# Optimization experiments

Measured on AMD Instinct MI355X. Metric: run time of the kernel, lower is better.

## Reference

```python
import jax, jax.numpy as jnp
import numpy as np

KSIZE = 3
STRIDE = 1
NEG_INF = -jnp.inf


def semiconv_maxmin(x, kernel, stride=STRIDE):
    """Tropical (max-min) 2D convolution, 'same' padding with -inf.

    out[n,o,i,j] = max over (c,kh,kw) of min(x_pad[n,c,i*s+kh,j*s+kw], kernel[o,c,kh,kw])
    """
    N, C, H, W = x.shape
    O, _, K, _ = kernel.shape
    p = K - 1
    top = p // 2
    bottom = p - top
    xp = jnp.pad(x, ((0, 0), (0, 0), (top, bottom), (top, bottom)),
                 constant_values=NEG_INF)
    Ho = (H + p - K) // stride + 1
    Wo = (W + p - K) // stride + 1
    out = jnp.full((N, O, Ho, Wo), NEG_INF, dtype=x.dtype)
    # Unrolled loop over the K*K taps (small, fixed); vectorized over n,o,c,h,w.
    for kh in range(K):
        for kw in range(K):
            xs = xp[:, :, kh:kh + stride * Ho:stride, kw:kw + stride * Wo:stride]  # [N,C,Ho,Wo]
            w = kernel[:, :, kh, kw]                                # [O,C]
            cand = jnp.minimum(xs[:, None], w[None, :, :, None, None])  # [N,O,C,Ho,Wo]
            out = jnp.maximum(out, jnp.max(cand, axis=2))
    return out


def setup_inputs() -> dict:
    key = jax.random.key(0)
    k1, k2 = jax.random.split(key)
    x = jax.random.normal(k1, (8, 32, 112, 112), dtype=jnp.float32)
    kernel = jax.random.normal(k2, (32, 32, KSIZE, KSIZE), dtype=jnp.float32)
    return {"x": x, "kernel": kernel}


def reference(x, kernel):
    return semiconv_maxmin(x, kernel, STRIDE)
```

## Files before the change

### kernel.cpp

```cpp
#include <hip/hip_runtime.h>
#include <math.h>

#define C_IN  32
#define O_OUT 32
#define HIMG  112
#define WIMG  112
#define HW    (HIMG * WIMG)
#define TS    8
#define NCP   16
#define XROW  12
#define XPLANE (10 * XROW)
#define WSLOT 12
#define OSTRIDE 196
#define NW    (O_OUT * NCP * WSLOT)

typedef _Float16 h2 __attribute__((ext_vector_type(2)));

static __device__ __forceinline__ h2 h2min(h2 a, h2 b) {
    return __builtin_elementwise_min(a, b);
}
static __device__ __forceinline__ h2 h2max(h2 a, h2 b) {
    return __builtin_elementwise_max(a, b);
}
static __device__ __forceinline__ h2 asH2(float f) {
    union { float f; h2 h; } u; u.f = f; return u.h;
}

__global__ void prep_weights(const float* __restrict__ kern, h2* __restrict__ wp)
{
    int idx = blockIdx.x * 256 + threadIdx.x;
    if (idx >= NW) return;
    int k  = idx % WSLOT;
    int cp = (idx / WSLOT) & (NCP - 1);
    int o  = idx / (WSLOT * NCP);
    float a = -INFINITY, b = -INFINITY;
    if (k < 9) {
        a = kern[(o * C_IN + 2 * cp    ) * 9 + k];
        b = kern[(o * C_IN + 2 * cp + 1) * 9 + k];
    }
    h2 v; v.x = (_Float16)a; v.y = (_Float16)b;
    wp[idx] = v;
}

__global__ __launch_bounds__(256, 4) void semiconv_kernel(
    const float* __restrict__ x, const h2* __restrict__ wp,
    float* __restrict__ out)
{
    __shared__ h2 xs[NCP * XPLANE];
    __shared__ h2 ws[O_OUT * OSTRIDE];

    const int tid = threadIdx.x;
    const int tj0 = blockIdx.x * TS;
    const int ti0 = blockIdx.y * TS;
    const int n   = blockIdx.z;
    const float* xn = x + (size_t)n * (C_IN * HW);

    #pragma unroll
    for (int i = 0; i < 6; ++i) {
        int chunk = i * 256 + tid;
        int o     = chunk / 48;
        int rem   = chunk - o * 48;
        float4 v  = *(const float4*)&wp[chunk * 4];
        *(float4*)&ws[o * OSTRIDE + rem * 4] = v;
    }
    #pragma unroll 1
    for (int idx = tid; idx < NCP * XPLANE; idx += 256) {
        int cp  = idx / XPLANE;
        int rem = idx - cp * XPLANE;
        int r   = rem / XROW;
        int col = rem - r * XROW;
        int gi = ti0 - 1 + r, gj = tj0 - 1 + col;
        float a = -INFINITY, b = -INFINITY;
        if (col < 10 && (unsigned)gi < (unsigned)HIMG && (unsigned)gj < (unsigned)WIMG) {
            const float* p = xn + (size_t)(2 * cp) * HW + gi * WIMG + gj;
            a = p[0];
            b = p[HW];
        }
        h2 v; v.x = (_Float16)a; v.y = (_Float16)b;
        xs[idx] = v;
    }
    __syncthreads();

    const int lane = tid & 63;
    const int wv   = tid >> 6;
    const int oL   = lane >> 3;
    const int pr   = lane & 7;
    const int o    = wv * 8 + oL;

    h2 ninf2; ninf2.x = (_Float16)(-INFINITY); ninf2.y = (_Float16)(-INFINITY);
    h2 acc[8];
    #pragma unroll
    for (int i = 0; i < 8; ++i) acc[i] = ninf2;

    #pragma unroll 2
    for (int cp = 0; cp < NCP; ++cp) {
        h2 xr[3][10];
        #pragma unroll
        for (int kh = 0; kh < 3; ++kh) {
            const h2* rp = &xs[cp * XPLANE + (pr + kh) * XROW];
            float4 a = *(const float4*)rp;
            float4 b = *(const float4*)(rp + 4);
            float2 c = *(const float2*)(rp + 8);
            xr[kh][0] = asH2(a.x); xr[kh][1] = asH2(a.y);
            xr[kh][2] = asH2(a.z); xr[kh][3] = asH2(a.w);
            xr[kh][4] = asH2(b.x); xr[kh][5] = asH2(b.y);
            xr[kh][6] = asH2(b.z); xr[kh][7] = asH2(b.w);
            xr[kh][8] = asH2(c.x); xr[kh][9] = asH2(c.y);
        }
        const h2* wq = &ws[o * OSTRIDE + cp * WSLOT];
        float4 wa = *(const float4*)wq;
        float4 wb = *(const float4*)(wq + 4);
        float  wc = *(const float*)(wq + 8);
        h2 w0 = asH2(wa.x), w1 = asH2(wa.y), w2 = asH2(wa.z), w3 = asH2(wa.w);
        h2 w4 = asH2(wb.x), w5 = asH2(wb.y), w6 = asH2(wb.z), w7 = asH2(wb.w);
        h2 w8 = asH2(wc);

        #pragma unroll
        for (int j = 0; j < 8; ++j) {
            h2 t0 = h2min(xr[0][j    ], w0);
            h2 t1 = h2min(xr[0][j + 1], w1);
            h2 t2 = h2min(xr[0][j + 2], w2);
            h2 t3 = h2min(xr[1][j    ], w3);
            h2 t4 = h2min(xr[1][j + 1], w4);
            h2 t5 = h2min(xr[1][j + 2], w5);
            h2 t6 = h2min(xr[2][j    ], w6);
            h2 t7 = h2min(xr[2][j + 1], w7);
            h2 t8 = h2min(xr[2][j + 2], w8);
            h2 r0 = h2max(h2max(t0, t1), t2);
            h2 r1 = h2max(h2max(t3, t4), t5);
            h2 r2 = h2max(h2max(t6, t7), t8);
            acc[j] = h2max(acc[j], h2max(h2max(r0, r1), r2));
        }
    }

    float* op = out + (((size_t)n * O_OUT + o) * HIMG + (ti0 + pr)) * WIMG + tj0;
    float4 v0, v1;
    v0.x = (float)(acc[0].x > acc[0].y ? acc[0].x : acc[0].y);
    v0.y = (float)(acc[1].x > acc[1].y ? acc[1].x : acc[1].y);
    v0.z = (float)(acc[2].x > acc[2].y ? acc[2].x : acc[2].y);
    v0.w = (float)(acc[3].x > acc[3].y ? acc[3].x : acc[3].y);
    v1.x = (float)(acc[4].x > acc[4].y ? acc[4].x : acc[4].y);
    v1.y = (float)(acc[5].x > acc[5].y ? acc[5].x : acc[5].y);
    v1.z = (float)(acc[6].x > acc[6].y ? acc[6].x : acc[6].y);
    v1.w = (float)(acc[7].x > acc[7].y ? acc[7].x : acc[7].y);
    *(float4*)op = v0;
    *(float4*)(op + 4) = v1;
}

extern "C" void kernel_launch(void* const* d_in, const int* in_sizes, int n_in,
                              void* d_out, int out_size, void* d_ws, size_t ws_size,
                              hipStream_t stream) {
    const float* x    = (const float*)d_in[0];
    const float* kern = (const float*)d_in[1];
    float* out        = (float*)d_out;
    h2* wp            = (h2*)d_ws;

    prep_weights<<<dim3((NW + 255) / 256), dim3(256), 0, stream>>>(kern, wp);
    dim3 grid(WIMG / TS, HIMG / TS, 8);
    semiconv_kernel<<<grid, dim3(256), 0, stream>>>(x, wp, out);
}
```

Before: 59.59 us.

## Split output channels across blocks and input channels across waves with LDS reduction

The grid is doubled so each block handles half of the output channels, which halves the weight tile in shared memory. Inside a block, the four waves are regrouped so that two waves split the input-channel pairs, and their partial max accumulators are merged through shared memory before the store. Launch bounds are raised to 8 blocks per CU for higher occupancy. The cost is that each input tile is now loaded and converted twice, once per output half, and an extra barrier and LDS round-trip are added.

```diff
diff --git a/kernel.cpp b/kernel.cpp
--- a/kernel.cpp
+++ b/kernel.cpp
@@ -12,6 +12,7 @@
 #define XPLANE (10 * XROW)
 #define WSLOT 12
 #define OSTRIDE 196
+#define OBLK  16
 #define NW    (O_OUT * NCP * WSLOT)
 
 typedef _Float16 h2 __attribute__((ext_vector_type(2)));
@@ -24,6 +25,9 @@
 }
 static __device__ __forceinline__ h2 asH2(float f) {
     union { float f; h2 h; } u; u.f = f; return u.h;
+}
+static __device__ __forceinline__ float asF(h2 h) {
+    union { h2 h; float f; } u; u.h = h; return u.f;
 }
 
 __global__ void prep_weights(const float* __restrict__ kern, h2* __restrict__ wp)
@@ -42,26 +46,27 @@
     wp[idx] = v;
 }
 
-__global__ __launch_bounds__(256, 4) void semiconv_kernel(
+__global__ __launch_bounds__(256, 8) void semiconv_kernel(
     const float* __restrict__ x, const h2* __restrict__ wp,
     float* __restrict__ out)
 {
     __shared__ h2 xs[NCP * XPLANE];
-    __shared__ h2 ws[O_OUT * OSTRIDE];
+    __shared__ h2 ws[OBLK * OSTRIDE];
 
     const int tid = threadIdx.x;
     const int tj0 = blockIdx.x * TS;
     const int ti0 = blockIdx.y * TS;
-    const int n   = blockIdx.z;
+    const int n   = blockIdx.z >> 1;
+    const int o0  = (blockIdx.z & 1) * OBLK;
     const float* xn = x + (size_t)n * (C_IN * HW);
 
     #pragma unroll
-    for (int i = 0; i < 6; ++i) {
+    for (int i = 0; i < 3; ++i) {
         int chunk = i * 256 + tid;
-        int o     = chunk / 48;
-        int rem   = chunk - o * 48;
-        float4 v  = *(const float4*)&wp[chunk * 4];
-        *(float4*)&ws[o * OSTRIDE + rem * 4] = v;
+        int oL    = chunk / 48;
+        int rem   = chunk - oL * 48;
+        float4 v  = *(const float4*)&wp[(size_t)((o0 + oL) * 48 + rem) * 4];
+        *(float4*)&ws[oL * OSTRIDE + rem * 4] = v;
     }
     #pragma unroll 1
     for (int idx = tid; idx < NCP * XPLANE; idx += 256) {
@@ -85,7 +90,10 @@
     const int wv   = tid >> 6;
     const int oL   = lane >> 3;
     const int pr   = lane & 7;
-    const int o    = wv * 8 + oL;
+    const int osl  = wv & 1;
+    const int cph  = wv >> 1;
+    const int oLoc = osl * 8 + oL;
+    const int o    = o0 + oLoc;
 
     h2 ninf2; ninf2.x = (_Float16)(-INFINITY); ninf2.y = (_Float16)(-INFINITY);
     h2 acc[8];
@@ -93,7 +101,8 @@
     for (int i = 0; i < 8; ++i) acc[i] = ninf2;
 
     #pragma unroll 2
-    for (int cp = 0; cp < NCP; ++cp) {
+    for (int ci = 0; ci < 8; ++ci) {
+        const int cp = cph * 8 + ci;
         h2 xr[3][10];
         #pragma unroll
         for (int kh = 0; kh < 3; ++kh) {
@@ -107,7 +116,7 @@
             xr[kh][6] = asH2(b.z); xr[kh][7] = asH2(b.w);
             xr[kh][8] = asH2(c.x); xr[kh][9] = asH2(c.y);
         }
-        const h2* wq = &ws[o * OSTRIDE + cp * WSLOT];
+        const h2* wq = &ws[oLoc * OSTRIDE + cp * WSLOT];
         float4 wa = *(const float4*)wq;
         float4 wb = *(const float4*)(wq + 4);
         float  wc = *(const float*)(wq + 8);
@@ -133,18 +142,40 @@
         }
     }
 
-    float* op = out + (((size_t)n * O_OUT + o) * HIMG + (ti0 + pr)) * WIMG + tj0;
-    float4 v0, v1;
-    v0.x = (float)(acc[0].x > acc[0].y ? acc[0].x : acc[0].y);
-    v0.y = (float)(acc[1].x > acc[1].y ? acc[1].x : acc[1].y);
-    v0.z = (float)(acc[2].x > acc[2].y ? acc[2].x : acc[2].y);
-    v0.w = (float)(acc[3].x > acc[3].y ? acc[3].x : acc[3].y);
-    v1.x = (float)(acc[4].x > acc[4].y ? acc[4].x : acc[4].y);
-    v1.y = (float)(acc[5].x > acc[5].y ? acc[5].x : acc[5].y);
-    v1.z = (float)(acc[6].x > acc[6].y ? acc[6].x : acc[6].y);
-    v1.w = (float)(acc[7].x > acc[7].y ? acc[7].x : acc[7].y);
-    *(float4*)op = v0;
-    *(float4*)(op + 4) = v1;
+    const int scr = oLoc * OSTRIDE + 96 + pr * 8;
+    if (cph == 1) {
+        float4 pa, pb;
+        pa.x = asF(acc[0]); pa.y = asF(acc[1]); pa.z = asF(acc[2]); pa.w = asF(acc[3]);
+        pb.x = asF(acc[4]); pb.y = asF(acc[5]); pb.z = asF(acc[6]); pb.w = asF(acc[7]);
+        *(float4*)&ws[scr]     = pa;
+        *(float4*)&ws[scr + 4] = pb;
+    }
+    __syncthreads();
+    if (cph == 0) {
+        float4 pa = *(const float4*)&ws[scr];
+        float4 pb = *(const float4*)&ws[scr + 4];
+        acc[0] = h2max(acc[0], asH2(pa.x));
+        acc[1] = h2max(acc[1], asH2(pa.y));
+        acc[2] = h2max(acc[2], asH2(pa.z));
+        acc[3] = h2max(acc[3], asH2(pa.w));
+        acc[4] = h2max(acc[4], asH2(pb.x));
+        acc[5] = h2max(acc[5], asH2(pb.y));
+        acc[6] = h2max(acc[6], asH2(pb.z));
+        acc[7] = h2max(acc[7], asH2(pb.w));
+
+        float* op = out + (((size_t)n * O_OUT + o) * HIMG + (ti0 + pr)) * WIMG + tj0;
+        float4 v0, v1;
+        v0.x = (float)(acc[0].x > acc[0].y ? acc[0].x : acc[0].y);
+        v0.y = (float)(acc[1].x > acc[1].y ? acc[1].x : acc[1].y);
+        v0.z = (float)(acc[2].x > acc[2].y ? acc[2].x : acc[2].y);
+        v0.w = (float)(acc[3].x > acc[3].y ? acc[3].x : acc[3].y);
+        v1.x = (float)(acc[4].x > acc[4].y ? acc[4].x : acc[4].y);
+        v1.y = (float)(acc[5].x > acc[5].y ? acc[5].x : acc[5].y);
+        v1.z = (float)(acc[6].x > acc[6].y ? acc[6].x : acc[6].y);
+        v1.w = (float)(acc[7].x > acc[7].y ? acc[7].x : acc[7].y);
+        *(float4*)op       = v0;
+        *(float4*)(op + 4) = v1;
+    }
 }
 
 extern "C" void kernel_launch(void* const* d_in, const int* in_sizes, int n_in,
@@ -156,6 +187,6 @@
     h2* wp            = (h2*)d_ws;
 
     prep_weights<<<dim3((NW + 255) / 256), dim3(256), 0, stream>>>(kern, wp);
-    dim3 grid(WIMG / TS, HIMG / TS, 8);
+    dim3 grid(WIMG / TS, HIMG / TS, 8 * 2);
     semiconv_kernel<<<grid, dim3(256), 0, stream>>>(x, wp, out);
 }
```

New measurement: 62.04 us. 4.1% more time.

## Split output channels across blocks and channels across waves with LDS reduction

Applied to the files above, without the earlier changes.

Each block now handles 16 output channels instead of 32, which doubles the grid along z. Within a block the four waves split the 16 input-channel pairs, and each thread computes two output rows so one set of loaded input rows is reused for both. The per-wave partial maxima are then reduced through shared memory, reusing the weight buffer. Launch bounds rise to allow 6 blocks per SM. The change adds an extra barrier and reduction step, the input tile is now loaded twice (once per output-channel half), and only wave 0 writes output.

```diff
diff --git a/kernel.cpp b/kernel.cpp
--- a/kernel.cpp
+++ b/kernel.cpp
@@ -11,7 +11,8 @@
 #define XROW  12
 #define XPLANE (10 * XROW)
 #define WSLOT 12
-#define OSTRIDE 196
+#define WSTRIDE 196
+#define OBLK  16
 #define NW    (O_OUT * NCP * WSLOT)
 
 typedef _Float16 h2 __attribute__((ext_vector_type(2)));
@@ -24,6 +25,9 @@
 }
 static __device__ __forceinline__ h2 asH2(float f) {
     union { float f; h2 h; } u; u.f = f; return u.h;
+}
+static __device__ __forceinline__ float asF(h2 h) {
+    union { h2 h; float f; } u; u.h = h; return u.f;
 }
 
 __global__ void prep_weights(const float* __restrict__ kern, h2* __restrict__ wp)
@@ -42,26 +46,27 @@
     wp[idx] = v;
 }
 
-__global__ __launch_bounds__(256, 4) void semiconv_kernel(
+__global__ __launch_bounds__(256, 6) void semiconv_kernel(
     const float* __restrict__ x, const h2* __restrict__ wp,
     float* __restrict__ out)
 {
     __shared__ h2 xs[NCP * XPLANE];
-    __shared__ h2 ws[O_OUT * OSTRIDE];
+    __shared__ h2 ws[OBLK * WSTRIDE];
 
     const int tid = threadIdx.x;
     const int tj0 = blockIdx.x * TS;
     const int ti0 = blockIdx.y * TS;
-    const int n   = blockIdx.z;
+    const int n   = blockIdx.z >> 1;
+    const int o0  = (blockIdx.z & 1) * OBLK;
     const float* xn = x + (size_t)n * (C_IN * HW);
 
     #pragma unroll
-    for (int i = 0; i < 6; ++i) {
+    for (int i = 0; i < 3; ++i) {
         int chunk = i * 256 + tid;
-        int o     = chunk / 48;
-        int rem   = chunk - o * 48;
-        float4 v  = *(const float4*)&wp[chunk * 4];
-        *(float4*)&ws[o * OSTRIDE + rem * 4] = v;
+        int oL    = chunk / 48;
+        int rem   = chunk - oL * 48;
+        float4 v  = *(const float4*)&wp[(size_t)((o0 + oL) * 48 + rem) * 4];
+        *(float4*)&ws[oL * WSTRIDE + rem * 4] = v;
     }
     #pragma unroll 1
     for (int idx = tid; idx < NCP * XPLANE; idx += 256) {
@@ -83,31 +88,34 @@
 
     const int lane = tid & 63;
     const int wv   = tid >> 6;
-    const int oL   = lane >> 3;
-    const int pr   = lane & 7;
-    const int o    = wv * 8 + oL;
+    const int oL   = lane & 15;
+    const int prg  = lane >> 4;
+    const int o    = o0 + oL;
 
     h2 ninf2; ninf2.x = (_Float16)(-INFINITY); ninf2.y = (_Float16)(-INFINITY);
-    h2 acc[8];
+    h2 acc[2][8];
     #pragma unroll
-    for (int i = 0; i < 8; ++i) acc[i] = ninf2;
+    for (int rr = 0; rr < 2; ++rr)
+        #pragma unroll
+        for (int j = 0; j < 8; ++j) acc[rr][j] = ninf2;
 
     #pragma unroll 2
-    for (int cp = 0; cp < NCP; ++cp) {
-        h2 xr[3][10];
-        #pragma unroll
-        for (int kh = 0; kh < 3; ++kh) {
-            const h2* rp = &xs[cp * XPLANE + (pr + kh) * XROW];
+    for (int ci = 0; ci < 4; ++ci) {
+        const int cp = wv * 4 + ci;
+        h2 xr[4][10];
+        #pragma unroll
+        for (int q = 0; q < 4; ++q) {
+            const h2* rp = &xs[cp * XPLANE + (2 * prg + q) * XROW];
             float4 a = *(const float4*)rp;
             float4 b = *(const float4*)(rp + 4);
             float2 c = *(const float2*)(rp + 8);
-            xr[kh][0] = asH2(a.x); xr[kh][1] = asH2(a.y);
-            xr[kh][2] = asH2(a.z); xr[kh][3] = asH2(a.w);
-            xr[kh][4] = asH2(b.x); xr[kh][5] = asH2(b.y);
-            xr[kh][6] = asH2(b.z); xr[kh][7] = asH2(b.w);
-            xr[kh][8] = asH2(c.x); xr[kh][9] = asH2(c.y);
-        }
-        const h2* wq = &ws[o * OSTRIDE + cp * WSLOT];
+            xr[q][0] = asH2(a.x); xr[q][1] = asH2(a.y);
+            xr[q][2] = asH2(a.z); xr[q][3] = asH2(a.w);
+            xr[q][4] = asH2(b.x); xr[q][5] = asH2(b.y);
+            xr[q][6] = asH2(b.z); xr[q][7] = asH2(b.w);
+            xr[q][8] = asH2(c.x); xr[q][9] = asH2(c.y);
+        }
+        const h2* wq = &ws[oL * WSTRIDE + cp * WSLOT];
         float4 wa = *(const float4*)wq;
         float4 wb = *(const float4*)(wq + 4);
         float  wc = *(const float*)(wq + 8);
@@ -116,35 +124,72 @@
         h2 w8 = asH2(wc);
 
         #pragma unroll
-        for (int j = 0; j < 8; ++j) {
-            h2 t0 = h2min(xr[0][j    ], w0);
-            h2 t1 = h2min(xr[0][j + 1], w1);
-            h2 t2 = h2min(xr[0][j + 2], w2);
-            h2 t3 = h2min(xr[1][j    ], w3);
-            h2 t4 = h2min(xr[1][j + 1], w4);
-            h2 t5 = h2min(xr[1][j + 2], w5);
-            h2 t6 = h2min(xr[2][j    ], w6);
-            h2 t7 = h2min(xr[2][j + 1], w7);
-            h2 t8 = h2min(xr[2][j + 2], w8);
-            h2 r0 = h2max(h2max(t0, t1), t2);
-            h2 r1 = h2max(h2max(t3, t4), t5);
-            h2 r2 = h2max(h2max(t6, t7), t8);
-            acc[j] = h2max(acc[j], h2max(h2max(r0, r1), r2));
-        }
-    }
-
-    float* op = out + (((size_t)n * O_OUT + o) * HIMG + (ti0 + pr)) * WIMG + tj0;
-    float4 v0, v1;
-    v0.x = (float)(acc[0].x > acc[0].y ? acc[0].x : acc[0].y);
-    v0.y = (float)(acc[1].x > acc[1].y ? acc[1].x : acc[1].y);
-    v0.z = (float)(acc[2].x > acc[2].y ? acc[2].x : acc[2].y);
-    v0.w = (float)(acc[3].x > acc[3].y ? acc[3].x : acc[3].y);
-    v1.x = (float)(acc[4].x > acc[4].y ? acc[4].x : acc[4].y);
-    v1.y = (float)(acc[5].x > acc[5].y ? acc[5].x : acc[5].y);
-    v1.z = (float)(acc[6].x > acc[6].y ? acc[6].x : acc[6].y);
-    v1.w = (float)(acc[7].x > acc[7].y ? acc[7].x : acc[7].y);
-    *(float4*)op = v0;
-    *(float4*)(op + 4) = v1;
+        for (int rr = 0; rr < 2; ++rr) {
+            #pragma unroll
+            for (int j = 0; j < 8; ++j) {
+                h2 t0 = h2min(xr[rr    ][j    ], w0);
+                h2 t1 = h2min(xr[rr    ][j + 1], w1);
+                h2 t2 = h2min(xr[rr    ][j + 2], w2);
+                h2 t3 = h2min(xr[rr + 1][j    ], w3);
+                h2 t4 = h2min(xr[rr + 1][j + 1], w4);
+                h2 t5 = h2min(xr[rr + 1][j + 2], w5);
+                h2 t6 = h2min(xr[rr + 2][j    ], w6);
+                h2 t7 = h2min(xr[rr + 2][j + 1], w7);
+                h2 t8 = h2min(xr[rr + 2][j + 2], w8);
+                h2 r0 = h2max(h2max(t0, t1), t2);
+                h2 r1 = h2max(h2max(t3, t4), t5);
+                h2 r2 = h2max(h2max(t6, t7), t8);
+                acc[rr][j] = h2max(acc[rr][j], h2max(h2max(r0, r1), r2));
+            }
+        }
+    }
+
+    __syncthreads();
+    if (wv != 0) {
+        h2* dst = &ws[(wv - 1) * 1024 + lane * 16];
+        float4 p0, p1, p2, p3;
+        p0.x = asF(acc[0][0]); p0.y = asF(acc[0][1]); p0.z = asF(acc[0][2]); p0.w = asF(acc[0][3]);
+        p1.x = asF(acc[0][4]); p1.y = asF(acc[0][5]); p1.z = asF(acc[0][6]); p1.w = asF(acc[0][7]);
+        p2.x = asF(acc[1][0]); p2.y = asF(acc[1][1]); p2.z = asF(acc[1][2]); p2.w = asF(acc[1][3]);
+        p3.x = asF(acc[1][4]); p3.y = asF(acc[1][5]); p3.z = asF(acc[1][6]); p3.w = asF(acc[1][7]);
+        ((float4*)dst)[0] = p0; ((float4*)dst)[1] = p1;
+        ((float4*)dst)[2] = p2; ((float4*)dst)[3] = p3;
+    }
+    __syncthreads();
+    if (wv == 0) {
+        #pragma unroll
+        for (int r = 0; r < 3; ++r) {
+            const h2* src = &ws[r * 1024 + lane * 16];
+            #pragma unroll
+            for (int half = 0; half < 2; ++half) {
+                float4 pa = ((const float4*)src)[half * 2];
+                float4 pb = ((const float4*)src)[half * 2 + 1];
+                acc[half][0] = h2max(acc[half][0], asH2(pa.x));
+                acc[half][1] = h2max(acc[half][1], asH2(pa.y));
+                acc[half][2] = h2max(acc[half][2], asH2(pa.z));
+                acc[half][3] = h2max(acc[half][3], asH2(pa.w));
+                acc[half][4] = h2max(acc[half][4], asH2(pb.x));
+                acc[half][5] = h2max(acc[half][5], asH2(pb.y));
+                acc[half][6] = h2max(acc[half][6], asH2(pb.z));
+                acc[half][7] = h2max(acc[half][7], asH2(pb.w));
+            }
+        }
+        float* op = out + (((size_t)n * O_OUT + o) * HIMG + (ti0 + 2 * prg)) * WIMG + tj0;
+        #pragma unroll
+        for (int rr = 0; rr < 2; ++rr) {
+            float4 v0, v1;
+            v0.x = (float)(acc[rr][0].x > acc[rr][0].y ? acc[rr][0].x : acc[rr][0].y);
+            v0.y = (float)(acc[rr][1].x > acc[rr][1].y ? acc[rr][1].x : acc[rr][1].y);
+            v0.z = (float)(acc[rr][2].x > acc[rr][2].y ? acc[rr][2].x : acc[rr][2].y);
+            v0.w = (float)(acc[rr][3].x > acc[rr][3].y ? acc[rr][3].x : acc[rr][3].y);
+            v1.x = (float)(acc[rr][4].x > acc[rr][4].y ? acc[rr][4].x : acc[rr][4].y);
+            v1.y = (float)(acc[rr][5].x > acc[rr][5].y ? acc[rr][5].x : acc[rr][5].y);
+            v1.z = (float)(acc[rr][6].x > acc[rr][6].y ? acc[rr][6].x : acc[rr][6].y);
+            v1.w = (float)(acc[rr][7].x > acc[rr][7].y ? acc[rr][7].x : acc[rr][7].y);
+            *(float4*)(op + rr * WIMG)     = v0;
+            *(float4*)(op + rr * WIMG + 4) = v1;
+        }
+    }
 }
 
 extern "C" void kernel_launch(void* const* d_in, const int* in_sizes, int n_in,
@@ -156,6 +201,6 @@
     h2* wp            = (h2*)d_ws;
 
     prep_weights<<<dim3((NW + 255) / 256), dim3(256), 0, stream>>>(kern, wp);
-    dim3 grid(WIMG / TS, HIMG / TS, 8);
+    dim3 grid(WIMG / TS, HIMG / TS, 8 * 2);
     semiconv_kernel<<<grid, dim3(256), 0, stream>>>(x, wp, out);
 }
```

Result: slower. 61.76 us (+3.6%).
